# Kernel optimization log

Hardware: AMD Instinct MI355X
Metric: run time of the kernel (lower is better)

## Reference

```python
import jax, jax.numpy as jnp
import numpy as np

E, D, H = 8, 512, 2048  # num_experts, features, features*mlp_ratio
B, S = 4, 512


def _lecun(key, shape):
    fan_in = shape[-2] if len(shape) >= 2 else shape[0]
    return jax.random.normal(key, shape, dtype=jnp.float32) / jnp.sqrt(jnp.float32(fan_in))


def setup_inputs() -> dict:
    key = jax.random.key(0)
    ks = jax.random.split(key, 8)
    return {
        'x_real': jax.random.normal(ks[0], (B, S, D), dtype=jnp.float32),
        'x_imag': jax.random.normal(ks[1], (B, S, D), dtype=jnp.float32),
        # gating Dense over concat([amp, phase]) -> in_features = 2*D
        'gate_W': _lecun(ks[2], (2 * D, E)),
        'gate_b': jnp.zeros((E,), jnp.float32),
        # per-expert ComplexLinear 1: D -> H
        'W1r': _lecun(ks[3], (E, D, H)),
        'W1i': _lecun(ks[4], (E, D, H)),
        'b1r': jnp.zeros((E, H), jnp.float32),
        'b1i': jnp.zeros((E, H), jnp.float32),
        # per-expert ComplexModReLU bias
        'mod_b': jnp.zeros((E, H), jnp.float32),
        # per-expert ComplexLinear 2: H -> D
        'W2r': _lecun(ks[5], (E, H, D)),
        'W2i': _lecun(ks[6], (E, H, D)),
        'b2r': jnp.zeros((E, D), jnp.float32),
        'b2i': jnp.zeros((E, D), jnp.float32),
    }


def reference(x_real, x_imag, gate_W, gate_b, W1r, W1i, b1r, b1i, mod_b, W2r, W2i, b2r, b2i):
    eps = 1e-10
    # --- gating: scores over [|z|, angle(z)] ---
    amp = jnp.sqrt(x_real ** 2 + x_imag ** 2)            # |z|, [B,S,D]
    phase = jnp.arctan2(x_imag, x_real)                  # angle(z)
    routing_input = jnp.concatenate([amp, phase], axis=-1)  # [B,S,2D]
    scores = routing_input @ gate_W + gate_b             # [B,S,E]
    probs = jax.nn.softmax(scores, axis=-1)
    idx = jnp.argmax(probs, axis=-1)                     # [B,S] top-1 expert

    # --- all experts dense (faithful to reference): complex linear 1 ---
    # (Wr + iWi)(xr + ixi) : hr = xr Wr - xi Wi ; hi = xr Wi + xi Wr
    h_r = (jnp.einsum('bsd,edh->ebsh', x_real, W1r)
           - jnp.einsum('bsd,edh->ebsh', x_imag, W1i)) + b1r[:, None, None, :]
    h_i = (jnp.einsum('bsd,edh->ebsh', x_real, W1i)
           + jnp.einsum('bsd,edh->ebsh', x_imag, W1r)) + b1i[:, None, None, :]

    # --- ComplexModReLU: relu(|z|+b) * z / (|z|+eps), |z| = sqrt(r^2+i^2+eps) ---
    a = jnp.sqrt(h_r ** 2 + h_i ** 2 + eps)              # [E,B,S,H]
    scale = jax.nn.relu(a + mod_b[:, None, None, :]) / (a + eps)
    h_r = h_r * scale
    h_i = h_i * scale

    # --- complex linear 2 ---
    o_r = (jnp.einsum('ebsh,ehd->ebsd', h_r, W2r)
           - jnp.einsum('ebsh,ehd->ebsd', h_i, W2i)) + b2r[:, None, None, :]
    o_i = (jnp.einsum('ebsh,ehd->ebsd', h_r, W2i)
           + jnp.einsum('ebsh,ehd->ebsd', h_i, W2r)) + b2i[:, None, None, :]

    # --- mask + weight (top-1): out = sum_e out_e * probs[...,e] * (argmax==e) ---
    e_ids = jnp.arange(probs.shape[-1])
    w = jnp.transpose(probs, (2, 0, 1)) * (idx[None, :, :] == e_ids[:, None, None])  # [E,B,S]
    out_r = jnp.einsum('ebs,ebsd->bsd', w, o_r)
    out_i = jnp.einsum('ebs,ebsd->bsd', w, o_i)
    return (out_r, out_i)
```

## Files before the change

kernel.cpp:

```cpp
#include <hip/hip_runtime.h>
#include <math.h>

#define NE 8
#define ND 512
#define NH 2048
#define NT 2048

typedef __attribute__((ext_vector_type(8))) short short8;
typedef __attribute__((ext_vector_type(4))) float f32x4;

#define GLL(g, d) __builtin_amdgcn_global_load_lds( \
    (const __attribute__((address_space(1))) void*)(g), \
    (__attribute__((address_space(3))) void*)(d), 16, 0, 0)

__device__ __forceinline__ unsigned short f2bf(float x) {
    unsigned int u = __builtin_bit_cast(unsigned int, x);
    u += 0x7FFFu + ((u >> 16) & 1u);
    return (unsigned short)(u >> 16);
}

__device__ __forceinline__ short8 lds8(const unsigned short* p) {
    return *(const short8*)p;
}

__global__ __launch_bounds__(256) void gate_kernel(
    const float* __restrict__ xr, const float* __restrict__ xi,
    const float* __restrict__ gW, const float* __restrict__ gb,
    float* __restrict__ gate_w,
    int* __restrict__ counts, int* __restrict__ tok_list,
    unsigned short* __restrict__ obr, unsigned short* __restrict__ obi)
{
    int t = blockIdx.x;
    int tid = threadIdx.x;
    const float* xrt = xr + (size_t)t * ND;
    const float* xit = xi + (size_t)t * ND;

    #pragma unroll
    for (int d = tid; d < ND; d += 256) {
        obr[(size_t)t * ND + d] = f2bf(xrt[d]);
        obi[(size_t)t * ND + d] = f2bf(xit[d]);
    }

    float acc[NE] = {0,0,0,0,0,0,0,0};
    for (int r = tid; r < 2 * ND; r += 256) {
        int d = r & (ND - 1);
        float a = xrt[d], b = xit[d];
        float v = (r < ND) ? sqrtf(a * a + b * b) : atan2f(b, a);
        const float4* g = (const float4*)(gW + (size_t)r * NE);
        float4 g0 = g[0], g1 = g[1];
        acc[0] += v * g0.x; acc[1] += v * g0.y; acc[2] += v * g0.z; acc[3] += v * g0.w;
        acc[4] += v * g1.x; acc[5] += v * g1.y; acc[6] += v * g1.z; acc[7] += v * g1.w;
    }
    #pragma unroll
    for (int e = 0; e < NE; e++) {
        for (int off = 32; off > 0; off >>= 1)
            acc[e] += __shfl_down(acc[e], off, 64);
    }
    __shared__ float part[4][NE];
    int wave = tid >> 6, lane = tid & 63;
    if (lane == 0) {
        #pragma unroll
        for (int e = 0; e < NE; e++) part[wave][e] = acc[e];
    }
    __syncthreads();
    if (tid == 0) {
        float s[NE];
        #pragma unroll
        for (int e = 0; e < NE; e++)
            s[e] = part[0][e] + part[1][e] + part[2][e] + part[3][e] + gb[e];
        int amax = 0; float m = s[0];
        #pragma unroll
        for (int e = 1; e < NE; e++) if (s[e] > m) { m = s[e]; amax = e; }
        float denom = 0.f;
        #pragma unroll
        for (int e = 0; e < NE; e++) denom += expf(s[e] - m);
        gate_w[t] = 1.0f / denom;
        int pos = atomicAdd(&counts[amax], 1);
        tok_list[amax * NT + pos] = t;
    }
}

__global__ void sched_kernel(const int* __restrict__ counts,
                             int* __restrict__ items, int* __restrict__ nitems)
{
    if (threadIdx.x == 0) {
        int k = 0;
        for (int e = 0; e < NE; e++) {
            int n = counts[e];
            int mt = (n + 63) >> 6;
            for (int m = 0; m < mt; m++) items[k++] = (e << 16) | m;
        }
        nitems[0] = k;
    }
}

__global__ __launch_bounds__(256) void transw_kernel(
    const float* __restrict__ s0, unsigned short* __restrict__ d0,
    const float* __restrict__ s1, unsigned short* __restrict__ d1,
    int R, int C)
{
    __shared__ float tile[64][65];
    int e = blockIdx.z;
    int c0 = blockIdx.x * 64, r0 = blockIdx.y * 64;
    size_t off = (size_t)e * R * C;
    int tid = threadIdx.x;
    #pragma unroll
    for (int p = 0; p < 2; ++p) {
        const float* src = (p ? s1 : s0) + off;
        unsigned short* dst = (p ? d1 : d0) + off;
        if (p) __syncthreads();
        for (int i = 0; i < 16; ++i) {
            int idx = tid + i * 256;
            int r = idx >> 6, c = idx & 63;
            tile[r][c] = src[(size_t)(r0 + r) * C + c0 + c];
        }
        __syncthreads();
        #pragma unroll
        for (int i = 0; i < 4; ++i) {
            int c = i * 16 + (tid >> 4);
            int r4 = (tid & 15) * 4;
            ushort4 v = make_ushort4(f2bf(tile[r4][c]), f2bf(tile[r4 + 1][c]),
                                     f2bf(tile[r4 + 2][c]), f2bf(tile[r4 + 3][c]));
            *(ushort4*)&dst[(size_t)(c0 + c) * R + r0 + r4] = v;
        }
    }
}


#define STAGE_(SA_R, SA_I, SB_R, SB_I, ko) do {  \
    GLL(gAr0 + (ko), SA_R + (w * 16) * 64);      \
    GLL(gAi0 + (ko), SA_I + (w * 16) * 64);      \
    GLL(gAr1 + (ko), SA_R + (w * 16 + 8) * 64);  \
    GLL(gAi1 + (ko), SA_I + (w * 16 + 8) * 64);  \
    GLL(gBr0 + (ko), SB_R + (w * 16) * 64);      \
    GLL(gBr1 + (ko), SB_R + (w * 16 + 8) * 64);  \
    GLL(gBi0 + (ko), SB_I + (w * 16) * 64);      \
    GLL(gBi1 + (ko), SB_I + (w * 16 + 8) * 64);  \
} while (0)

#define COMPUTE_(SA_R, SA_I, SB_R, SB_I) do {                                          \
    _Pragma("unroll")                                                                  \
    for (int ks = 0; ks < 2; ++ks) {                                                   \
        int pa = ((ks * 4 + quad) ^ (l15 & 7)) * 8;                                    \
        short8 br  = lds8(SB_R + (w * 16 + l15) * 64 + pa);                            \
        short8 bi2 = lds8(SB_I + (w * 16 + l15) * 64 + pa);                            \
        _Pragma("unroll")                                                              \
        for (int m = 0; m < 4; ++m) {                                                  \
            short8 ar  = lds8(SA_R + (m * 16 + l15) * 64 + pa);                        \
            short8 ai2 = lds8(SA_I + (m * 16 + l15) * 64 + pa);                        \
            aRR[m] = __builtin_amdgcn_mfma_f32_16x16x32_bf16(ar,  br,  aRR[m], 0, 0, 0); \
            aII[m] = __builtin_amdgcn_mfma_f32_16x16x32_bf16(ai2, bi2, aII[m], 0, 0, 0); \
            aRI[m] = __builtin_amdgcn_mfma_f32_16x16x32_bf16(ar,  bi2, aRI[m], 0, 0, 0); \
            aIR[m] = __builtin_amdgcn_mfma_f32_16x16x32_bf16(ai2, br,  aIR[m], 0, 0, 0); \
        }                                                                              \
    }                                                                                  \
} while (0)

#define VMW8  asm volatile("s_waitcnt vmcnt(8)" ::: "memory")
#define VMW0  asm volatile("s_waitcnt vmcnt(0)" ::: "memory")
#define BARX do {                            \
    __builtin_amdgcn_sched_barrier(0);       \
    __builtin_amdgcn_s_barrier();            \
    __builtin_amdgcn_sched_barrier(0);       \
} while (0)

#define MOE_LDS_DECL                                                        \
    __shared__ alignas(16) unsigned short sAr0[4096], sAi0[4096];           \
    __shared__ alignas(16) unsigned short sBr0[4096], sBi0[4096];           \
    __shared__ alignas(16) unsigned short sAr1[4096], sAi1[4096];           \
    __shared__ alignas(16) unsigned short sBr1[4096], sBi1[4096];

#define PIPE_LOOP(NK) do {                                                  \
    STAGE_(sAr0, sAi0, sBr0, sBi0, 0);                                      \
    VMW0; BARX;                                                             \
    _Pragma("unroll 1")                                                     \
    for (int kt = 0; kt < (NK); kt += 2) {                                  \
        if (kt + 1 < (NK)) { STAGE_(sAr1, sAi1, sBr1, sBi1, (kt + 1) * 64); VMW8; } \
        else VMW0;                                                          \
        BARX;                                                               \
        COMPUTE_(sAr0, sAi0, sBr0, sBi0);                                   \
        BARX;                                                               \
        if (kt + 2 < (NK)) { STAGE_(sAr0, sAi0, sBr0, sBi0, (kt + 2) * 64); VMW8; } \
        else VMW0;                                                          \
        BARX;                                                               \
        COMPUTE_(sAr1, sAi1, sBr1, sBi1);                                   \
        BARX;                                                               \
    }                                                                       \
} while (0)

#define NBLK 512

__global__ __launch_bounds__(256, 2) void moe1_kernel(
    const unsigned short* __restrict__ xbr, const unsigned short* __restrict__ xbi,
    const unsigned short* __restrict__ w1tr, const unsigned short* __restrict__ w1ti,
    const float* __restrict__ b1r, const float* __restrict__ b1i,
    const float* __restrict__ mod_b,
    const int* __restrict__ counts, const int* __restrict__ tok_list,
    const int* __restrict__ items, const int* __restrict__ nitems,
    unsigned short* __restrict__ hr, unsigned short* __restrict__ hi)
{
    int tid = threadIdx.x;
    int w = tid >> 6, l = tid & 63;
    int l15 = l & 15, quad = l >> 4;
    int swz = (((l & 7) ^ ((l >> 3) & 7)) * 8);

    MOE_LDS_DECL

    int total = nitems[0] * 32;
    int chunk = (total + NBLK - 1) / NBLK;
    int u0 = blockIdx.x * chunk;
    int u1 = u0 + chunk; if (u1 > total) u1 = total;

    for (int u = u0; u < u1; ++u) {
        int it = items[u >> 5];
        int nt = u & 31;
        int e = it >> 16, mt = it & 0xffff;
        int n = counts[e];
        int mbase = mt * 64, n0 = nt * 64;
        const int* tl = tok_list + e * NT;

        int ia0 = mbase + w * 16 + (l >> 3);
        int ia1 = ia0 + 8;
        int ra0 = tl[ia0 < n ? ia0 : n - 1];
        int ra1 = tl[ia1 < n ? ia1 : n - 1];
        const unsigned short* gAr0 = xbr + (size_t)ra0 * ND + swz;
        const unsigned short* gAi0 = xbi + (size_t)ra0 * ND + swz;
        const unsigned short* gAr1 = xbr + (size_t)ra1 * ND + swz;
        const unsigned short* gAi1 = xbi + (size_t)ra1 * ND + swz;
        size_t brow = (size_t)e * NH + n0 + w * 16 + (l >> 3);
        const unsigned short* gBr0 = w1tr + brow * ND + swz;
        const unsigned short* gBr1 = w1tr + (brow + 8) * ND + swz;
        const unsigned short* gBi0 = w1ti + brow * ND + swz;
        const unsigned short* gBi1 = w1ti + (brow + 8) * ND + swz;

        f32x4 aRR[4] = {}, aII[4] = {}, aRI[4] = {}, aIR[4] = {};

        PIPE_LOOP(ND / 64);

        int col = n0 + w * 16 + l15;
        float bre = b1r[(size_t)e * NH + col];
        float bie = b1i[(size_t)e * NH + col];
        float mbv = mod_b[(size_t)e * NH + col];
        #pragma unroll
        for (int m = 0; m < 4; ++m) {
            #pragma unroll
            for (int r = 0; r < 4; ++r) {
                int tix = m * 16 + quad * 4 + r;
                if (mbase + tix >= n) continue;
                int tok = tl[mbase + tix];
                float vr = aRR[m][r] - aII[m][r] + bre;
                float vi = aRI[m][r] + aIR[m][r] + bie;
                float a = sqrtf(vr * vr + vi * vi + 1e-10f);
                float sc = fmaxf(a + mbv, 0.0f) / (a + 1e-10f);
                hr[(size_t)tok * NH + col] = f2bf(vr * sc);
                hi[(size_t)tok * NH + col] = f2bf(vi * sc);
            }
        }
    }
}

__global__ __launch_bounds__(256, 2) void moe2_kernel(
    const unsigned short* __restrict__ hr, const unsigned short* __restrict__ hi,
    const unsigned short* __restrict__ w2tr, const unsigned short* __restrict__ w2ti,
    const float* __restrict__ b2r, const float* __restrict__ b2i,
    const int* __restrict__ counts, const int* __restrict__ tok_list,
    const int* __restrict__ items, const int* __restrict__ nitems,
    const float* __restrict__ gate_w,
    float* __restrict__ out)
{
    int tid = threadIdx.x;
    int w = tid >> 6, l = tid & 63;
    int l15 = l & 15, quad = l >> 4;
    int swz = (((l & 7) ^ ((l >> 3) & 7)) * 8);

    MOE_LDS_DECL

    int total = nitems[0] * 8;
    int chunk = (total + NBLK - 1) / NBLK;
    int u0 = blockIdx.x * chunk;
    int u1 = u0 + chunk; if (u1 > total) u1 = total;

    for (int u = u0; u < u1; ++u) {
        int it = items[u >> 3];
        int nt = u & 7;
        int e = it >> 16, mt = it & 0xffff;
        int n = counts[e];
        int mbase = mt * 64, n0 = nt * 64;
        const int* tl = tok_list + e * NT;

        int ia0 = mbase + w * 16 + (l >> 3);
        int ia1 = ia0 + 8;
        int ra0 = tl[ia0 < n ? ia0 : n - 1];
        int ra1 = tl[ia1 < n ? ia1 : n - 1];
        const unsigned short* gAr0 = hr + (size_t)ra0 * NH + swz;
        const unsigned short* gAi0 = hi + (size_t)ra0 * NH + swz;
        const unsigned short* gAr1 = hr + (size_t)ra1 * NH + swz;
        const unsigned short* gAi1 = hi + (size_t)ra1 * NH + swz;
        size_t brow = (size_t)e * ND + n0 + w * 16 + (l >> 3);
        const unsigned short* gBr0 = w2tr + brow * NH + swz;
        const unsigned short* gBr1 = w2tr + (brow + 8) * NH + swz;
        const unsigned short* gBi0 = w2ti + brow * NH + swz;
        const unsigned short* gBi1 = w2ti + (brow + 8) * NH + swz;

        f32x4 aRR[4] = {}, aII[4] = {}, aRI[4] = {}, aIR[4] = {};

        PIPE_LOOP(NH / 64);

        int col = n0 + w * 16 + l15;
        float bre = b2r[(size_t)e * ND + col];
        float bie = b2i[(size_t)e * ND + col];
        #pragma unroll
        for (int m = 0; m < 4; ++m) {
            #pragma unroll
            for (int r = 0; r < 4; ++r) {
                int tix = m * 16 + quad * 4 + r;
                if (mbase + tix >= n) continue;
                int tok = tl[mbase + tix];
                float gw = gate_w[tok];
                out[(size_t)tok * ND + col] = (aRR[m][r] - aII[m][r] + bre) * gw;
                out[(size_t)NT * ND + (size_t)tok * ND + col] = (aRI[m][r] + aIR[m][r] + bie) * gw;
            }
        }
    }
}

extern "C" void kernel_launch(void* const* d_in, const int* in_sizes, int n_in,
                              void* d_out, int out_size, void* d_ws, size_t ws_size,
                              hipStream_t stream) {
    const float* xr   = (const float*)d_in[0];
    const float* xi   = (const float*)d_in[1];
    const float* gW   = (const float*)d_in[2];
    const float* gb   = (const float*)d_in[3];
    const float* W1r  = (const float*)d_in[4];
    const float* W1i  = (const float*)d_in[5];
    const float* b1r  = (const float*)d_in[6];
    const float* b1i  = (const float*)d_in[7];
    const float* modb = (const float*)d_in[8];
    const float* W2r  = (const float*)d_in[9];
    const float* W2i  = (const float*)d_in[10];
    const float* b2r  = (const float*)d_in[11];
    const float* b2i  = (const float*)d_in[12];
    float* out = (float*)d_out;

    char* ws = (char*)d_ws;
    int*   counts   = (int*)ws;
    float* gate_w   = (float*)(ws + 256);
    int*   tok_list = (int*)(ws + 256 + 8192);
    size_t off = 256 + 8192 + (size_t)NE * NT * 4;
    int*   items    = (int*)(ws + off); off += 256;
    int*   nitems   = (int*)(ws + off); off += 256;
    unsigned short* xbr  = (unsigned short*)(ws + off); off += (size_t)NT * ND * 2;
    unsigned short* xbi  = (unsigned short*)(ws + off); off += (size_t)NT * ND * 2;
    unsigned short* w1tr = (unsigned short*)(ws + off); off += (size_t)NE * ND * NH * 2;
    unsigned short* w1ti = (unsigned short*)(ws + off); off += (size_t)NE * ND * NH * 2;
    unsigned short* w2tr = (unsigned short*)(ws + off); off += (size_t)NE * ND * NH * 2;
    unsigned short* w2ti = (unsigned short*)(ws + off); off += (size_t)NE * ND * NH * 2;
    unsigned short* h_r  = (unsigned short*)(ws + off); off += (size_t)NT * NH * 2;
    unsigned short* h_i  = (unsigned short*)(ws + off); off += (size_t)NT * NH * 2;

    hipMemsetAsync(counts, 0, 64 * sizeof(int), stream);
    gate_kernel<<<NT, 256, 0, stream>>>(xr, xi, gW, gb, gate_w, counts, tok_list, xbr, xbi);
    sched_kernel<<<1, 64, 0, stream>>>(counts, items, nitems);
    transw_kernel<<<dim3(NH / 64, ND / 64, NE), 256, 0, stream>>>(W1r, w1tr, W1i, w1ti, ND, NH);
    transw_kernel<<<dim3(ND / 64, NH / 64, NE), 256, 0, stream>>>(W2r, w2tr, W2i, w2ti, NH, ND);
    moe1_kernel<<<NBLK, 256, 0, stream>>>(
        xbr, xbi, w1tr, w1ti, b1r, b1i, modb, counts, tok_list, items, nitems, h_r, h_i);
    moe2_kernel<<<NBLK, 256, 0, stream>>>(
        h_r, h_i, w2tr, w2ti, b2r, b2i, counts, tok_list, items, nitems, gate_w, out);
}
```

Measured before the change: 311.3 us.

## Drop schedule kernel and memset, launch one block per tile, vectorize weight transpose

Removes the single-thread schedule kernel and the memset. Counts are now zeroed inside the first transpose launch, and each MoE block finds its (expert, m-tile) item by scanning counts, using a fixed grid sized for the worst case (MAXIT tiles) in place of a persistent chunked loop. The weight transpose now does float4 loads and converts to bf16 before writing LDS, then stores 16-byte rows. The MFMA compute sections also raise wave priority with setprio. The aim is fewer launches and serialized tiny kernels, plus better load balance and transpose bandwidth. The cost is many idle blocks that exit early, and a hard limit of 40 tiles: with 2048 tokens over 8 experts the worst case is 39 tiles, so it fits.

```diff
diff --git a/kernel.cpp b/kernel.cpp
--- a/kernel.cpp
+++ b/kernel.cpp
@@ -5,6 +5,7 @@
 #define ND 512
 #define NH 2048
 #define NT 2048
+#define MAXIT 40
 
 typedef __attribute__((ext_vector_type(8))) short short8;
 typedef __attribute__((ext_vector_type(4))) float f32x4;
@@ -80,26 +81,15 @@
     }
 }
 
-__global__ void sched_kernel(const int* __restrict__ counts,
-                             int* __restrict__ items, int* __restrict__ nitems)
-{
-    if (threadIdx.x == 0) {
-        int k = 0;
-        for (int e = 0; e < NE; e++) {
-            int n = counts[e];
-            int mt = (n + 63) >> 6;
-            for (int m = 0; m < mt; m++) items[k++] = (e << 16) | m;
-        }
-        nitems[0] = k;
-    }
-}
-
 __global__ __launch_bounds__(256) void transw_kernel(
     const float* __restrict__ s0, unsigned short* __restrict__ d0,
     const float* __restrict__ s1, unsigned short* __restrict__ d1,
-    int R, int C)
+    int R, int C, int* __restrict__ counts, int zero_counts)
 {
-    __shared__ float tile[64][65];
+    __shared__ unsigned short t[64][72];
+    if (zero_counts && blockIdx.x == 0 && blockIdx.y == 0 && blockIdx.z == 0
+        && threadIdx.x < 16)
+        counts[threadIdx.x] = 0;
     int e = blockIdx.z;
     int c0 = blockIdx.x * 64, r0 = blockIdx.y * 64;
     size_t off = (size_t)e * R * C;
@@ -109,19 +99,23 @@
         const float* src = (p ? s1 : s0) + off;
         unsigned short* dst = (p ? d1 : d0) + off;
         if (p) __syncthreads();
-        for (int i = 0; i < 16; ++i) {
-            int idx = tid + i * 256;
-            int r = idx >> 6, c = idx & 63;
-            tile[r][c] = src[(size_t)(r0 + r) * C + c0 + c];
+        #pragma unroll
+        for (int i = 0; i < 4; ++i) {
+            int r = i * 16 + (tid >> 4);
+            int c4 = (tid & 15) * 4;
+            float4 v = *(const float4*)&src[(size_t)(r0 + r) * C + c0 + c4];
+            t[c4 + 0][r] = f2bf(v.x);
+            t[c4 + 1][r] = f2bf(v.y);
+            t[c4 + 2][r] = f2bf(v.z);
+            t[c4 + 3][r] = f2bf(v.w);
         }
         __syncthreads();
         #pragma unroll
-        for (int i = 0; i < 4; ++i) {
-            int c = i * 16 + (tid >> 4);
-            int r4 = (tid & 15) * 4;
-            ushort4 v = make_ushort4(f2bf(tile[r4][c]), f2bf(tile[r4 + 1][c]),
-                                     f2bf(tile[r4 + 2][c]), f2bf(tile[r4 + 3][c]));
-            *(ushort4*)&dst[(size_t)(c0 + c) * R + r0 + r4] = v;
+        for (int i = 0; i < 2; ++i) {
+            int c = i * 32 + (tid >> 3);
+            int r8 = (tid & 7) * 8;
+            short8 v = *(const short8*)&t[c][r8];
+            *(short8*)&dst[(size_t)(c0 + c) * R + r0 + r8] = v;
         }
     }
 }
@@ -178,17 +172,31 @@
         if (kt + 1 < (NK)) { STAGE_(sAr1, sAi1, sBr1, sBi1, (kt + 1) * 64); VMW8; } \
         else VMW0;                                                          \
         BARX;                                                               \
+        __builtin_amdgcn_s_setprio(1);                                      \
         COMPUTE_(sAr0, sAi0, sBr0, sBi0);                                   \
+        __builtin_amdgcn_s_setprio(0);                                      \
         BARX;                                                               \
         if (kt + 2 < (NK)) { STAGE_(sAr0, sAi0, sBr0, sBi0, (kt + 2) * 64); VMW8; } \
         else VMW0;                                                          \
         BARX;                                                               \
+        __builtin_amdgcn_s_setprio(1);                                      \
         COMPUTE_(sAr1, sAi1, sBr1, sBi1);                                   \
+        __builtin_amdgcn_s_setprio(0);                                      \
         BARX;                                                               \
     }                                                                       \
 } while (0)
 
-#define NBLK 512
+__device__ __forceinline__ bool find_item(const int* counts, int item,
+                                          int& e, int& mt, int& n) {
+    int rem = item;
+    for (e = 0; e < NE; ++e) {
+        n = counts[e];
+        int m = (n + 63) >> 6;
+        if (rem < m) { mt = rem; return true; }
+        rem -= m;
+    }
+    return false;
+}
 
 __global__ __launch_bounds__(256, 2) void moe1_kernel(
     const unsigned short* __restrict__ xbr, const unsigned short* __restrict__ xbi,
@@ -196,9 +204,13 @@
     const float* __restrict__ b1r, const float* __restrict__ b1i,
     const float* __restrict__ mod_b,
     const int* __restrict__ counts, const int* __restrict__ tok_list,
-    const int* __restrict__ items, const int* __restrict__ nitems,
     unsigned short* __restrict__ hr, unsigned short* __restrict__ hi)
 {
+    int e, mt, n;
+    if (!find_item(counts, blockIdx.x >> 5, e, mt, n)) return;
+    int nt = blockIdx.x & 31;
+    int mbase = mt * 64, n0 = nt * 64;
+
     int tid = threadIdx.x;
     int w = tid >> 6, l = tid & 63;
     int l15 = l & 15, quad = l >> 4;
@@ -206,55 +218,42 @@
 
     MOE_LDS_DECL
 
-    int total = nitems[0] * 32;
-    int chunk = (total + NBLK - 1) / NBLK;
-    int u0 = blockIdx.x * chunk;
-    int u1 = u0 + chunk; if (u1 > total) u1 = total;
-
-    for (int u = u0; u < u1; ++u) {
-        int it = items[u >> 5];
-        int nt = u & 31;
-        int e = it >> 16, mt = it & 0xffff;
-        int n = counts[e];
-        int mbase = mt * 64, n0 = nt * 64;
-        const int* tl = tok_list + e * NT;
-
-        int ia0 = mbase + w * 16 + (l >> 3);
-        int ia1 = ia0 + 8;
-        int ra0 = tl[ia0 < n ? ia0 : n - 1];
-        int ra1 = tl[ia1 < n ? ia1 : n - 1];
-        const unsigned short* gAr0 = xbr + (size_t)ra0 * ND + swz;
-        const unsigned short* gAi0 = xbi + (size_t)ra0 * ND + swz;
-        const unsigned short* gAr1 = xbr + (size_t)ra1 * ND + swz;
-        const unsigned short* gAi1 = xbi + (size_t)ra1 * ND + swz;
-        size_t brow = (size_t)e * NH + n0 + w * 16 + (l >> 3);
-        const unsigned short* gBr0 = w1tr + brow * ND + swz;
-        const unsigned short* gBr1 = w1tr + (brow + 8) * ND + swz;
-        const unsigned short* gBi0 = w1ti + brow * ND + swz;
-        const unsigned short* gBi1 = w1ti + (brow + 8) * ND + swz;
-
-        f32x4 aRR[4] = {}, aII[4] = {}, aRI[4] = {}, aIR[4] = {};
-
-        PIPE_LOOP(ND / 64);
-
-        int col = n0 + w * 16 + l15;
-        float bre = b1r[(size_t)e * NH + col];
-        float bie = b1i[(size_t)e * NH + col];
-        float mbv = mod_b[(size_t)e * NH + col];
-        #pragma unroll
-        for (int m = 0; m < 4; ++m) {
-            #pragma unroll
-            for (int r = 0; r < 4; ++r) {
-                int tix = m * 16 + quad * 4 + r;
-                if (mbase + tix >= n) continue;
-                int tok = tl[mbase + tix];
-                float vr = aRR[m][r] - aII[m][r] + bre;
-                float vi = aRI[m][r] + aIR[m][r] + bie;
-                float a = sqrtf(vr * vr + vi * vi + 1e-10f);
-                float sc = fmaxf(a + mbv, 0.0f) / (a + 1e-10f);
-                hr[(size_t)tok * NH + col] = f2bf(vr * sc);
-                hi[(size_t)tok * NH + col] = f2bf(vi * sc);
-            }
+    const int* tl = tok_list + e * NT;
+    int ia0 = mbase + w * 16 + (l >> 3);
+    int ia1 = ia0 + 8;
+    int ra0 = tl[ia0 < n ? ia0 : n - 1];
+    int ra1 = tl[ia1 < n ? ia1 : n - 1];
+    const unsigned short* gAr0 = xbr + (size_t)ra0 * ND + swz;
+    const unsigned short* gAi0 = xbi + (size_t)ra0 * ND + swz;
+    const unsigned short* gAr1 = xbr + (size_t)ra1 * ND + swz;
+    const unsigned short* gAi1 = xbi + (size_t)ra1 * ND + swz;
+    size_t brow = (size_t)e * NH + n0 + w * 16 + (l >> 3);
+    const unsigned short* gBr0 = w1tr + brow * ND + swz;
+    const unsigned short* gBr1 = w1tr + (brow + 8) * ND + swz;
+    const unsigned short* gBi0 = w1ti + brow * ND + swz;
+    const unsigned short* gBi1 = w1ti + (brow + 8) * ND + swz;
+
+    f32x4 aRR[4] = {}, aII[4] = {}, aRI[4] = {}, aIR[4] = {};
+
+    PIPE_LOOP(ND / 64);
+
+    int col = n0 + w * 16 + l15;
+    float bre = b1r[(size_t)e * NH + col];
+    float bie = b1i[(size_t)e * NH + col];
+    float mbv = mod_b[(size_t)e * NH + col];
+    #pragma unroll
+    for (int m = 0; m < 4; ++m) {
+        #pragma unroll
+        for (int r = 0; r < 4; ++r) {
+            int tix = m * 16 + quad * 4 + r;
+            if (mbase + tix >= n) continue;
+            int tok = tl[mbase + tix];
+            float vr = aRR[m][r] - aII[m][r] + bre;
+            float vi = aRI[m][r] + aIR[m][r] + bie;
+            float a = sqrtf(vr * vr + vi * vi + 1e-10f);
+            float sc = fmaxf(a + mbv, 0.0f) / (a + 1e-10f);
+            hr[(size_t)tok * NH + col] = f2bf(vr * sc);
+            hi[(size_t)tok * NH + col] = f2bf(vi * sc);
         }
     }
 }
@@ -264,10 +263,14 @@
     const unsigned short* __restrict__ w2tr, const unsigned short* __restrict__ w2ti,
     const float* __restrict__ b2r, const float* __restrict__ b2i,
     const int* __restrict__ counts, const int* __restrict__ tok_list,
-    const int* __restrict__ items, const int* __restrict__ nitems,
     const float* __restrict__ gate_w,
     float* __restrict__ out)
 {
+    int e, mt, n;
+    if (!find_item(counts, blockIdx.x >> 3, e, mt, n)) return;
+    int nt = blockIdx.x & 7;
+    int mbase = mt * 64, n0 = nt * 64;
+
     int tid = threadIdx.x;
     int w = tid >> 6, l = tid & 63;
     int l15 = l & 15, quad = l >> 4;
@@ -275,51 +278,38 @@
 
     MOE_LDS_DECL
 
-    int total = nitems[0] * 8;
-    int chunk = (total + NBLK - 1) / NBLK;
-    int u0 = blockIdx.x * chunk;
-    int u1 = u0 + chunk; if (u1 > total) u1 = total;
-
-    for (int u = u0; u < u1; ++u) {
-        int it = items[u >> 3];
-        int nt = u & 7;
-        int e = it >> 16, mt = it & 0xffff;
-        int n = counts[e];
-        int mbase = mt * 64, n0 = nt * 64;
-        const int* tl = tok_list + e * NT;
-
-        int ia0 = mbase + w * 16 + (l >> 3);
-        int ia1 = ia0 + 8;
-        int ra0 = tl[ia0 < n ? ia0 : n - 1];
-        int ra1 = tl[ia1 < n ? ia1 : n - 1];
-        const unsigned short* gAr0 = hr + (size_t)ra0 * NH + swz;
-        const unsigned short* gAi0 = hi + (size_t)ra0 * NH + swz;
-        const unsigned short* gAr1 = hr + (size_t)ra1 * NH + swz;
-        const unsigned short* gAi1 = hi + (size_t)ra1 * NH + swz;
-        size_t brow = (size_t)e * ND + n0 + w * 16 + (l >> 3);
-        const unsigned short* gBr0 = w2tr + brow * NH + swz;
-        const unsigned short* gBr1 = w2tr + (brow + 8) * NH + swz;
-        const unsigned short* gBi0 = w2ti + brow * NH + swz;
-        const unsigned short* gBi1 = w2ti + (brow + 8) * NH + swz;
-
-        f32x4 aRR[4] = {}, aII[4] = {}, aRI[4] = {}, aIR[4] = {};
-
-        PIPE_LOOP(NH / 64);
-
-        int col = n0 + w * 16 + l15;
-        float bre = b2r[(size_t)e * ND + col];
-        float bie = b2i[(size_t)e * ND + col];
-        #pragma unroll
-        for (int m = 0; m < 4; ++m) {
-            #pragma unroll
-            for (int r = 0; r < 4; ++r) {
-                int tix = m * 16 + quad * 4 + r;
-                if (mbase + tix >= n) continue;
-                int tok = tl[mbase + tix];
-                float gw = gate_w[tok];
-                out[(size_t)tok * ND + col] = (aRR[m][r] - aII[m][r] + bre) * gw;
-                out[(size_t)NT * ND + (size_t)tok * ND + col] = (aRI[m][r] + aIR[m][r] + bie) * gw;
-            }
+    const int* tl = tok_list + e * NT;
+    int ia0 = mbase + w * 16 + (l >> 3);
+    int ia1 = ia0 + 8;
+    int ra0 = tl[ia0 < n ? ia0 : n - 1];
+    int ra1 = tl[ia1 < n ? ia1 : n - 1];
+    const unsigned short* gAr0 = hr + (size_t)ra0 * NH + swz;
+    const unsigned short* gAi0 = hi + (size_t)ra0 * NH + swz;
+    const unsigned short* gAr1 = hr + (size_t)ra1 * NH + swz;
+    const unsigned short* gAi1 = hi + (size_t)ra1 * NH + swz;
+    size_t brow = (size_t)e * ND + n0 + w * 16 + (l >> 3);
+    const unsigned short* gBr0 = w2tr + brow * NH + swz;
+    const unsigned short* gBr1 = w2tr + (brow + 8) * NH + swz;
+    const unsigned short* gBi0 = w2ti + brow * NH + swz;
+    const unsigned short* gBi1 = w2ti + (brow + 8) * NH + swz;
+
+    f32x4 aRR[4] = {}, aII[4] = {}, aRI[4] = {}, aIR[4] = {};
+
+    PIPE_LOOP(NH / 64);
+
+    int col = n0 + w * 16 + l15;
+    float bre = b2r[(size_t)e * ND + col];
+    float bie = b2i[(size_t)e * ND + col];
+    #pragma unroll
+    for (int m = 0; m < 4; ++m) {
+        #pragma unroll
+        for (int r = 0; r < 4; ++r) {
+            int tix = m * 16 + quad * 4 + r;
+            if (mbase + tix >= n) continue;
+            int tok = tl[mbase + tix];
+            float gw = gate_w[tok];
+            out[(size_t)tok * ND + col] = (aRR[m][r] - aII[m][r] + bre) * gw;
+            out[(size_t)NT * ND + (size_t)tok * ND + col] = (aRI[m][r] + aIR[m][r] + bie) * gw;
         }
     }
 }
@@ -347,8 +337,6 @@
     float* gate_w   = (float*)(ws + 256);
     int*   tok_list = (int*)(ws + 256 + 8192);
     size_t off = 256 + 8192 + (size_t)NE * NT * 4;
-    int*   items    = (int*)(ws + off); off += 256;
-    int*   nitems   = (int*)(ws + off); off += 256;
     unsigned short* xbr  = (unsigned short*)(ws + off); off += (size_t)NT * ND * 2;
     unsigned short* xbi  = (unsigned short*)(ws + off); off += (size_t)NT * ND * 2;
     unsigned short* w1tr = (unsigned short*)(ws + off); off += (size_t)NE * ND * NH * 2;
@@ -358,13 +346,13 @@
     unsigned short* h_r  = (unsigned short*)(ws + off); off += (size_t)NT * NH * 2;
     unsigned short* h_i  = (unsigned short*)(ws + off); off += (size_t)NT * NH * 2;
 
-    hipMemsetAsync(counts, 0, 64 * sizeof(int), stream);
+    transw_kernel<<<dim3(NH / 64, ND / 64, NE), 256, 0, stream>>>(
+        W1r, w1tr, W1i, w1ti, ND, NH, counts, 1);
+    transw_kernel<<<dim3(ND / 64, NH / 64, NE), 256, 0, stream>>>(
+        W2r, w2tr, W2i, w2ti, NH, ND, counts, 0);
     gate_kernel<<<NT, 256, 0, stream>>>(xr, xi, gW, gb, gate_w, counts, tok_list, xbr, xbi);
-    sched_kernel<<<1, 64, 0, stream>>>(counts, items, nitems);
-    transw_kernel<<<dim3(NH / 64, ND / 64, NE), 256, 0, stream>>>(W1r, w1tr, W1i, w1ti, ND, NH);
-    transw_kernel<<<dim3(ND / 64, NH / 64, NE), 256, 0, stream>>>(W2r, w2tr, W2i, w2ti, NH, ND);
-    moe1_kernel<<<NBLK, 256, 0, stream>>>(
-        xbr, xbi, w1tr, w1ti, b1r, b1i, modb, counts, tok_list, items, nitems, h_r, h_i);
-    moe2_kernel<<<NBLK, 256, 0, stream>>>(
-        h_r, h_i, w2tr, w2ti, b2r, b2i, counts, tok_list, items, nitems, gate_w, out);
-}
+    moe1_kernel<<<MAXIT * 32, 256, 0, stream>>>(
+        xbr, xbi, w1tr, w1ti, b1r, b1i, modb, counts, tok_list, h_r, h_i);
+    moe2_kernel<<<MAXIT * 8, 256, 0, stream>>>(
+        h_r, h_i, w2tr, w2ti, b2r, b2i, counts, tok_list, gate_w, out);
+}
```

Result: faster. 297.6 us (-4.4%).
